# Kernel tuning notes

Hardware: AMD Instinct MI355X
Metric: run time of the kernel (lower is better)

The kernel has to match this reference:

```python
import jax, jax.numpy as jnp
import numpy as np

D = 1024
HEAD_DIM = D // 16  # attention_heads=16, used only for the softmax scale


def setup_inputs() -> dict:
    key = jax.random.key(0)
    ks = jax.random.split(key, 9)
    s = 1.0 / np.sqrt(D)
    return {
        "features": jax.random.normal(ks[0], (4, 2048, D), dtype=jnp.float32),
        "Wq": jax.random.normal(ks[1], (D, D), dtype=jnp.float32) * s,
        "bq": jnp.zeros((D,), dtype=jnp.float32),
        "Wk": jax.random.normal(ks[2], (D, D), dtype=jnp.float32) * s,
        "bk": jnp.zeros((D,), dtype=jnp.float32),
        "Wv": jax.random.normal(ks[3], (D, D), dtype=jnp.float32) * s,
        "bv": jnp.zeros((D,), dtype=jnp.float32),
        "Wo": jax.random.normal(ks[4], (D, D), dtype=jnp.float32) * s,
        "bo": jnp.zeros((D,), dtype=jnp.float32),
    }


def reference(features, Wq, bq, Wk, bk, Wv, bv, Wo, bo):
    # torch nn.Linear: x @ W.T + b
    q = features @ Wq.T + bq  # [B, S, D]
    k = features @ Wk.T + bk
    v = features @ Wv.T + bv
    scale = 1.0 / np.sqrt(HEAD_DIM).astype(np.float32)
    scores = jnp.einsum("bsd,btd->bst", q, k) * scale  # [B, S, S]
    weights = jax.nn.softmax(scores, axis=-1)
    out = jnp.einsum("bst,btd->bsd", weights, v)
    return out @ Wo.T + bo
```

## Files before the change

kernel.cpp:

```cpp
#include <hip/hip_runtime.h>


using u16 = unsigned short;
typedef __bf16 bf16x8 __attribute__((ext_vector_type(8)));
typedef float f32x4 __attribute__((ext_vector_type(4)));

__device__ inline u16 f2bf(float f) {
  union { float f; unsigned int u; } c; c.f = f;
  unsigned int u = c.u;
  u += 0x7fffu + ((u >> 16) & 1u);
  return (u16)(u >> 16);
}

__global__ __launch_bounds__(256) void cast_all(
    const float4* __restrict__ feat, const float4* __restrict__ wq,
    const float4* __restrict__ wk, const float4* __restrict__ wv,
    const float4* __restrict__ wo, ushort4* __restrict__ xbf,
    ushort4* __restrict__ wcat, float* __restrict__ lsum) {
  const int b = blockIdx.x, tx = threadIdx.x;
  if (b >= 12288) {
    lsum[(b - 12288) * 256 + tx] = 0.f;
    return;
  }
  const float4* src; ushort4* dst; int idx;
  if (b < 8192) { src = feat; dst = xbf; idx = b * 256 + tx; }
  else {
    const int w = (b - 8192) >> 10, loc = ((b - 8192) & 1023) * 256 + tx;
    src = (w == 0) ? wq : (w == 1) ? wk : (w == 2) ? wv : wo;
    dst = wcat + w * 262144; idx = loc;
  }
  float4 v = src[idx];
  ushort4 o;
  o.x = f2bf(v.x); o.y = f2bf(v.y); o.z = f2bf(v.z); o.w = f2bf(v.w);
  dst[idx] = o;
}

template <int MODE>
__global__ __launch_bounds__(256) void gemm_bt(
    const u16* __restrict__ A, const u16* __restrict__ Bm, void* __restrict__ C,
    void* __restrict__ C2, void* __restrict__ C3,
    const float* __restrict__ bias, const float* __restrict__ bias2,
    const float* __restrict__ bias3, float* __restrict__ lsum,
    int M, int N, int K, int lda, int ldc,
    float scale,
    long long sA, long long sB, long long sC)
{
  __shared__ u16 As[128 * 64];
  __shared__ u16 Bs[128 * 64];
  const int tx = threadIdx.x;
  const int wave = tx >> 6, lane = tx & 63;
  const int wm = (wave >> 1) * 64, wn = (wave & 1) * 64;
  const int m0 = blockIdx.y * 128, n0 = blockIdx.x * 128;
  const u16* Ab = A + blockIdx.z * sA + (long long)m0 * lda;
  const u16* Bb = Bm + blockIdx.z * sB + (long long)n0 * K;

  f32x4 acc[4][4] = {};

  int rT[4], qT[4];
#pragma unroll
  for (int t = 0; t < 4; ++t) {
    rT[t] = t * 32 + wave * 8 + (lane >> 3);
    qT[t] = (((lane & 7) - rT[t]) & 7) << 3;
  }
  const int ldsT[4] = {wave * 512, 2048 + wave * 512, 4096 + wave * 512,
                       6144 + wave * 512};

  const int fr = lane & 15, fq = lane >> 4;

  for (int k0 = 0; k0 < K; k0 += 64) {
#pragma unroll
    for (int t = 0; t < 4; ++t) {
      __builtin_amdgcn_global_load_lds(
          (const __attribute__((address_space(1))) void*)(Ab + (long long)rT[t] * lda + k0 + qT[t]),
          (__attribute__((address_space(3))) void*)(As + ldsT[t]), 16, 0, 0);
      __builtin_amdgcn_global_load_lds(
          (const __attribute__((address_space(1))) void*)(Bb + (long long)rT[t] * K + k0 + qT[t]),
          (__attribute__((address_space(3))) void*)(Bs + ldsT[t]), 16, 0, 0);
    }
    __syncthreads();

#pragma unroll
    for (int s = 0; s < 2; ++s) {
      bf16x8 af[4], bfv[4];
#pragma unroll
      for (int i = 0; i < 4; ++i) {
        const int Ra = wm + i * 16 + fr;
        const int Rb = wn + i * 16 + fr;
        af[i]  = *(const bf16x8*)(As + Ra * 64 + (((s * 4 + fq + Ra) & 7) << 3));
        bfv[i] = *(const bf16x8*)(Bs + Rb * 64 + (((s * 4 + fq + Rb) & 7) << 3));
      }
#pragma unroll
      for (int i = 0; i < 4; ++i)
#pragma unroll
        for (int j = 0; j < 4; ++j)
          acc[i][j] = __builtin_amdgcn_mfma_f32_16x16x32_bf16(af[i], bfv[j], acc[i][j], 0, 0, 0);
    }
    __syncthreads();
  }

  const int col = lane & 15, rq = (lane >> 4) << 2;
  const long long zC = (long long)blockIdx.z * sC;

  if constexpr (MODE == 5) {
    float rsum[4][4] = {};
#pragma unroll
    for (int i = 0; i < 4; ++i) {
#pragma unroll
      for (int j = 0; j < 4; ++j) {
        const int gn = n0 + wn + j * 16 + col;
#pragma unroll
        for (int r = 0; r < 4; ++r) {
          const int gm = m0 + wm + i * 16 + rq + r;
          const float e = __expf(acc[i][j][r] * scale);
          ((u16*)C)[zC + (long long)gm * ldc + gn] = f2bf(e);
          rsum[i][r] += e;
        }
      }
    }
#pragma unroll
    for (int i = 0; i < 4; ++i) {
#pragma unroll
      for (int r = 0; r < 4; ++r) {
        float s = rsum[i][r];
        s += __shfl_xor(s, 1); s += __shfl_xor(s, 2);
        s += __shfl_xor(s, 4); s += __shfl_xor(s, 8);
        if (col == 0)
          atomicAdd(&lsum[(long long)blockIdx.z * 2048 + m0 + wm + i * 16 + rq + r], s);
      }
    }
  } else if constexpr (MODE == 4) {
    float inv[4][4];
#pragma unroll
    for (int i = 0; i < 4; ++i)
#pragma unroll
      for (int r = 0; r < 4; ++r)
        inv[i][r] = 1.0f / lsum[(long long)blockIdx.z * 2048 + m0 + wm + i * 16 + rq + r];
#pragma unroll
    for (int i = 0; i < 4; ++i)
#pragma unroll
      for (int j = 0; j < 4; ++j) {
        const int gn = n0 + wn + j * 16 + col;
#pragma unroll
        for (int r = 0; r < 4; ++r) {
          const int gm = m0 + wm + i * 16 + rq + r;
          ((u16*)C)[zC + (long long)gm * ldc + gn] = f2bf(acc[i][j][r] * inv[i][r]);
        }
      }
  } else if constexpr (MODE == 3) {
    const int sect = n0 >> 10;
#pragma unroll
    for (int i = 0; i < 4; ++i) {
#pragma unroll
      for (int j = 0; j < 4; ++j) {
        const int gn = n0 + wn + j * 16 + col;
        const int nb = gn & 1023;
        const float bv = (sect == 0) ? bias[nb] : (sect == 1) ? bias2[nb] : bias3[nb];
#pragma unroll
        for (int r = 0; r < 4; ++r) {
          const int gm = m0 + wm + i * 16 + rq + r;
          const float v = acc[i][j][r] + bv;
          if (sect == 0) {
            ((u16*)C)[(long long)gm * 1024 + nb] = f2bf(v);
          } else if (sect == 1) {
            ((u16*)C2)[(long long)gm * 1024 + nb] = f2bf(v);
          } else {
            const int bb = gm >> 11, t = gm & 2047;
            ((u16*)C3)[((long long)bb << 21) + (long long)nb * 2048 + t] = f2bf(v);
          }
        }
      }
    }
  } else {
#pragma unroll
    for (int i = 0; i < 4; ++i) {
#pragma unroll
      for (int j = 0; j < 4; ++j) {
        const int gn = n0 + wn + j * 16 + col;
        const float bv = bias[gn];
#pragma unroll
        for (int r = 0; r < 4; ++r) {
          const int gm = m0 + wm + i * 16 + rq + r;
          ((float*)C)[zC + (long long)gm * ldc + gn] = acc[i][j][r] + bv;
        }
      }
    }
  }
}

extern "C" void kernel_launch(void* const* d_in, const int* in_sizes, int n_in,
                              void* d_out, int out_size, void* d_ws, size_t ws_size,
                              hipStream_t stream) {
  (void)in_sizes; (void)n_in; (void)out_size; (void)ws_size;
  const float* feat = (const float*)d_in[0];
  const float* Wq = (const float*)d_in[1];
  const float* bq = (const float*)d_in[2];
  const float* Wk = (const float*)d_in[3];
  const float* bk = (const float*)d_in[4];
  const float* Wv = (const float*)d_in[5];
  const float* bv = (const float*)d_in[6];
  const float* Wo = (const float*)d_in[7];
  const float* bo = (const float*)d_in[8];
  float* out = (float*)d_out;

  char* ws = (char*)d_ws;
  const unsigned long long MB = 1024ull * 1024ull;
  u16* Xbf  = (u16*)(ws);
  u16* Wcat = (u16*)(ws + 16 * MB);
  u16* Wob  = Wcat + 3ll * 1024 * 1024;
  u16* Q    = (u16*)(ws + 24 * MB);
  u16* Kbuf = (u16*)(ws + 40 * MB);
  u16* Vt   = (u16*)(ws + 56 * MB);
  u16* P    = (u16*)(ws + 72 * MB);
  float* lsum = (float*)(ws + 104 * MB);
  u16* attn = Q;

  dim3 blk(256);

  cast_all<<<12320, blk, 0, stream>>>((const float4*)feat, (const float4*)Wq,
                                      (const float4*)Wk, (const float4*)Wv,
                                      (const float4*)Wo, (ushort4*)Xbf,
                                      (ushort4*)Wcat, lsum);

  gemm_bt<3><<<dim3(24, 64, 1), blk, 0, stream>>>(
      Xbf, Wcat, Q, Kbuf, Vt, bq, bk, bv, nullptr,
      8192, 3072, 1024, 1024, 0, 1.f, 0, 0, 0);

  gemm_bt<5><<<dim3(16, 16, 4), blk, 0, stream>>>(
      Q, Kbuf, P, nullptr, nullptr, nullptr, nullptr, nullptr, lsum,
      2048, 2048, 1024, 1024, 2048, 0.125f,
      2048ll * 1024, 2048ll * 1024, 2048ll * 2048);

  gemm_bt<4><<<dim3(8, 16, 4), blk, 0, stream>>>(
      P, Vt, attn, nullptr, nullptr, nullptr, nullptr, nullptr, lsum,
      2048, 1024, 2048, 2048, 1024, 1.f,
      2048ll * 2048, 1024ll * 2048, 2048ll * 1024);

  gemm_bt<2><<<dim3(8, 64, 1), blk, 0, stream>>>(
      attn, Wob, out, nullptr, nullptr, bo, nullptr, nullptr, nullptr,
      8192, 1024, 1024, 1024, 1024, 1.f, 0, 0, 0);
}
```

Baseline: 307.9 us.

## Rewrite GEMM as 8-wave 256-row tiles with double-buffered LDS prefetch

Replaces the 128x128 single-buffer GEMM with a 512-thread kernel that computes 256xBN tiles (BN 256 or 128 per call). Global-to-LDS loads are double buffered, with the next tiles' loads issued in quarters between MFMA phases and fenced by explicit vmcnt waits and barriers. MFMA sections run at raised wave priority. The aim is to hide global load latency behind compute and raise data reuse per block, at the cost of more LDS and registers per block and fewer blocks for the smaller attention GEMMs.

After: 346.0 us. 1.12x slower.

```diff
diff --git a/kernel.cpp b/kernel.cpp
--- a/kernel.cpp
+++ b/kernel.cpp
@@ -4,6 +4,9 @@
 using u16 = unsigned short;
 typedef __bf16 bf16x8 __attribute__((ext_vector_type(8)));
 typedef float f32x4 __attribute__((ext_vector_type(4)));
+
+#define AS1 __attribute__((address_space(1)))
+#define AS3 __attribute__((address_space(3)))
 
 __device__ inline u16 f2bf(float f) {
   union { float f; unsigned int u; } c; c.f = f;
@@ -35,153 +38,190 @@
   dst[idx] = o;
 }
 
-template <int MODE>
-__global__ __launch_bounds__(256) void gemm_bt(
+template <int MODE, int BN>
+__global__ __launch_bounds__(512, 2) void gemm8p(
     const u16* __restrict__ A, const u16* __restrict__ Bm, void* __restrict__ C,
     void* __restrict__ C2, void* __restrict__ C3,
     const float* __restrict__ bias, const float* __restrict__ bias2,
     const float* __restrict__ bias3, float* __restrict__ lsum,
-    int M, int N, int K, int lda, int ldc,
-    float scale,
+    int M, int N, int K, int lda, int ldc, float scale,
     long long sA, long long sB, long long sC)
 {
-  __shared__ u16 As[128 * 64];
-  __shared__ u16 Bs[128 * 64];
+  constexpr int NL  = BN / 128;
+  constexpr int NFH = BN / 128;
+  constexpr int NH  = BN / 2;
+  constexpr int NW  = NH / 4;
+
+  __shared__ u16 As[2 * 256 * 64];
+  __shared__ u16 Bs[2 * BN * 64];
+
   const int tx = threadIdx.x;
   const int wave = tx >> 6, lane = tx & 63;
-  const int wm = (wave >> 1) * 64, wn = (wave & 1) * 64;
-  const int m0 = blockIdx.y * 128, n0 = blockIdx.x * 128;
+  const int wm = wave >> 2, wn = wave & 3;
+  const int fr = lane & 15, fq = lane >> 4;
+  const int lr = lane >> 3, lp = lane & 7;
+  const int m0 = blockIdx.y * 256, n0 = blockIdx.x * BN;
   const u16* Ab = A + blockIdx.z * sA + (long long)m0 * lda;
   const u16* Bb = Bm + blockIdx.z * sB + (long long)n0 * K;
-
-  f32x4 acc[4][4] = {};
-
-  int rT[4], qT[4];
-#pragma unroll
-  for (int t = 0; t < 4; ++t) {
-    rT[t] = t * 32 + wave * 8 + (lane >> 3);
-    qT[t] = (((lane & 7) - rT[t]) & 7) << 3;
-  }
-  const int ldsT[4] = {wave * 512, 2048 + wave * 512, 4096 + wave * 512,
-                       6144 + wave * 512};
-
-  const int fr = lane & 15, fq = lane >> 4;
-
-  for (int k0 = 0; k0 < K; k0 += 64) {
-#pragma unroll
-    for (int t = 0; t < 4; ++t) {
+  const int NT = K >> 6;
+
+  f32x4 acc[8][2 * NFH] = {};
+
+  auto stageA = [&](int t, int h) {
+#pragma unroll
+    for (int s = 0; s < 2; ++s) {
+      const int R = h * 128 + wave * 16 + s * 8 + lr;
+      const int q = (lp - R) & 7;
       __builtin_amdgcn_global_load_lds(
-          (const __attribute__((address_space(1))) void*)(Ab + (long long)rT[t] * lda + k0 + qT[t]),
-          (__attribute__((address_space(3))) void*)(As + ldsT[t]), 16, 0, 0);
+          (const AS1 void*)(Ab + (long long)R * lda + t * 64 + q * 8),
+          (AS3 void*)(As + (t & 1) * 16384 + (h * 128 + wave * 16 + s * 8) * 64),
+          16, 0, 0);
+    }
+  };
+  auto stageB = [&](int t, int h) {
+#pragma unroll
+    for (int s = 0; s < NL; ++s) {
+      const int R = h * NH + wave * (8 * NL) + s * 8 + lr;
+      const int q = (lp - R) & 7;
       __builtin_amdgcn_global_load_lds(
-          (const __attribute__((address_space(1))) void*)(Bb + (long long)rT[t] * K + k0 + qT[t]),
-          (__attribute__((address_space(3))) void*)(Bs + ldsT[t]), 16, 0, 0);
-    }
-    __syncthreads();
-
-#pragma unroll
-    for (int s = 0; s < 2; ++s) {
-      bf16x8 af[4], bfv[4];
-#pragma unroll
-      for (int i = 0; i < 4; ++i) {
-        const int Ra = wm + i * 16 + fr;
-        const int Rb = wn + i * 16 + fr;
-        af[i]  = *(const bf16x8*)(As + Ra * 64 + (((s * 4 + fq + Ra) & 7) << 3));
-        bfv[i] = *(const bf16x8*)(Bs + Rb * 64 + (((s * 4 + fq + Rb) & 7) << 3));
-      }
-#pragma unroll
-      for (int i = 0; i < 4; ++i)
-#pragma unroll
-        for (int j = 0; j < 4; ++j)
-          acc[i][j] = __builtin_amdgcn_mfma_f32_16x16x32_bf16(af[i], bfv[j], acc[i][j], 0, 0, 0);
-    }
-    __syncthreads();
+          (const AS1 void*)(Bb + (long long)R * K + t * 64 + q * 8),
+          (AS3 void*)(Bs + (t & 1) * (BN * 64) + (h * NH + wave * (8 * NL) + s * 8) * 64),
+          16, 0, 0);
+    }
+  };
+
+  stageA(0, 0); stageA(0, 1); stageB(0, 0); stageB(0, 1);
+  stageA(1, 0); stageB(1, 0);
+  if constexpr (BN == 256) asm volatile("s_waitcnt vmcnt(4)" ::: "memory");
+  else                     asm volatile("s_waitcnt vmcnt(3)" ::: "memory");
+  __builtin_amdgcn_s_barrier();
+
+  for (int t = 0; t < NT; ++t) {
+    const u16* At = As + (t & 1) * 16384;
+    const u16* Bt = Bs + (t & 1) * (BN * 64);
+#pragma unroll
+    for (int qp = 0; qp < 4; ++qp) {
+      const int h = qp >> 1, g = qp & 1;
+      bf16x8 af[4][2], bv[NFH][2];
+#pragma unroll
+      for (int fi = 0; fi < 4; ++fi) {
+        const int R = h * 128 + wm * 64 + fi * 16 + fr;
+#pragma unroll
+        for (int s = 0; s < 2; ++s)
+          af[fi][s] = *(const bf16x8*)(At + R * 64 + (((s * 4 + fq + R) & 7) << 3));
+      }
+#pragma unroll
+      for (int fj = 0; fj < NFH; ++fj) {
+        const int R = g * NH + wn * NW + fj * 16 + fr;
+#pragma unroll
+        for (int s = 0; s < 2; ++s)
+          bv[fj][s] = *(const bf16x8*)(Bt + R * 64 + (((s * 4 + fq + R) & 7) << 3));
+      }
+      if (qp == 0)      { if (t + 1 < NT) stageA(t + 1, 1); }
+      else if (qp == 1) { if (t + 1 < NT) stageB(t + 1, 1); }
+      else if (qp == 2) { if (t + 2 < NT) stageA(t + 2, 0); }
+      else              { if (t + 2 < NT) stageB(t + 2, 0); }
+
+      __builtin_amdgcn_s_barrier();
+      asm volatile("s_waitcnt lgkmcnt(0)" ::: "memory");
+      __builtin_amdgcn_sched_barrier(0);
+      __builtin_amdgcn_s_setprio(1);
+#pragma unroll
+      for (int s = 0; s < 2; ++s)
+#pragma unroll
+        for (int fi = 0; fi < 4; ++fi)
+#pragma unroll
+          for (int fj = 0; fj < NFH; ++fj)
+            acc[h * 4 + fi][g * NFH + fj] = __builtin_amdgcn_mfma_f32_16x16x32_bf16(
+                af[fi][s], bv[fj][s], acc[h * 4 + fi][g * NFH + fj], 0, 0, 0);
+      __builtin_amdgcn_s_setprio(0);
+      if (qp == 3) {
+        if constexpr (BN == 256) asm volatile("s_waitcnt vmcnt(4)" ::: "memory");
+        else                     asm volatile("s_waitcnt vmcnt(3)" ::: "memory");
+      }
+      __builtin_amdgcn_s_barrier();
+    }
   }
 
   const int col = lane & 15, rq = (lane >> 4) << 2;
   const long long zC = (long long)blockIdx.z * sC;
 
   if constexpr (MODE == 5) {
-    float rsum[4][4] = {};
-#pragma unroll
-    for (int i = 0; i < 4; ++i) {
-#pragma unroll
-      for (int j = 0; j < 4; ++j) {
-        const int gn = n0 + wn + j * 16 + col;
+#pragma unroll
+    for (int i = 0; i < 8; ++i) {
+      const int gmb = m0 + (i >> 2) * 128 + wm * 64 + (i & 3) * 16 + rq;
+      float rs[4] = {0.f, 0.f, 0.f, 0.f};
+#pragma unroll
+      for (int j = 0; j < 2 * NFH; ++j) {
+        const int gn = n0 + (j / NFH) * NH + wn * NW + (j % NFH) * 16 + col;
 #pragma unroll
         for (int r = 0; r < 4; ++r) {
-          const int gm = m0 + wm + i * 16 + rq + r;
           const float e = __expf(acc[i][j][r] * scale);
-          ((u16*)C)[zC + (long long)gm * ldc + gn] = f2bf(e);
-          rsum[i][r] += e;
+          ((u16*)C)[zC + (long long)(gmb + r) * ldc + gn] = f2bf(e);
+          rs[r] += e;
         }
       }
-    }
-#pragma unroll
-    for (int i = 0; i < 4; ++i) {
 #pragma unroll
       for (int r = 0; r < 4; ++r) {
-        float s = rsum[i][r];
+        float s = rs[r];
         s += __shfl_xor(s, 1); s += __shfl_xor(s, 2);
         s += __shfl_xor(s, 4); s += __shfl_xor(s, 8);
         if (col == 0)
-          atomicAdd(&lsum[(long long)blockIdx.z * 2048 + m0 + wm + i * 16 + rq + r], s);
+          atomicAdd(&lsum[(long long)blockIdx.z * 2048 + gmb + r], s);
       }
     }
   } else if constexpr (MODE == 4) {
-    float inv[4][4];
-#pragma unroll
-    for (int i = 0; i < 4; ++i)
+#pragma unroll
+    for (int i = 0; i < 8; ++i) {
+      const int gmb = m0 + (i >> 2) * 128 + wm * 64 + (i & 3) * 16 + rq;
+      float inv[4];
 #pragma unroll
       for (int r = 0; r < 4; ++r)
-        inv[i][r] = 1.0f / lsum[(long long)blockIdx.z * 2048 + m0 + wm + i * 16 + rq + r];
-#pragma unroll
-    for (int i = 0; i < 4; ++i)
-#pragma unroll
-      for (int j = 0; j < 4; ++j) {
-        const int gn = n0 + wn + j * 16 + col;
-#pragma unroll
-        for (int r = 0; r < 4; ++r) {
-          const int gm = m0 + wm + i * 16 + rq + r;
-          ((u16*)C)[zC + (long long)gm * ldc + gn] = f2bf(acc[i][j][r] * inv[i][r]);
-        }
-      }
+        inv[r] = 1.0f / lsum[(long long)blockIdx.z * 2048 + gmb + r];
+#pragma unroll
+      for (int j = 0; j < 2 * NFH; ++j) {
+        const int gn = n0 + (j / NFH) * NH + wn * NW + (j % NFH) * 16 + col;
+#pragma unroll
+        for (int r = 0; r < 4; ++r)
+          ((u16*)C)[zC + (long long)(gmb + r) * ldc + gn] = f2bf(acc[i][j][r] * inv[r]);
+      }
+    }
   } else if constexpr (MODE == 3) {
     const int sect = n0 >> 10;
 #pragma unroll
-    for (int i = 0; i < 4; ++i) {
-#pragma unroll
-      for (int j = 0; j < 4; ++j) {
-        const int gn = n0 + wn + j * 16 + col;
+    for (int i = 0; i < 8; ++i) {
+      const int gmb = m0 + (i >> 2) * 128 + wm * 64 + (i & 3) * 16 + rq;
+#pragma unroll
+      for (int j = 0; j < 2 * NFH; ++j) {
+        const int gn = n0 + (j / NFH) * NH + wn * NW + (j % NFH) * 16 + col;
         const int nb = gn & 1023;
-        const float bv = (sect == 0) ? bias[nb] : (sect == 1) ? bias2[nb] : bias3[nb];
+        const float bvv = (sect == 0) ? bias[nb] : (sect == 1) ? bias2[nb] : bias3[nb];
 #pragma unroll
         for (int r = 0; r < 4; ++r) {
-          const int gm = m0 + wm + i * 16 + rq + r;
-          const float v = acc[i][j][r] + bv;
+          const int gm = gmb + r;
+          const float v = acc[i][j][r] + bvv;
           if (sect == 0) {
             ((u16*)C)[(long long)gm * 1024 + nb] = f2bf(v);
           } else if (sect == 1) {
             ((u16*)C2)[(long long)gm * 1024 + nb] = f2bf(v);
           } else {
-            const int bb = gm >> 11, t = gm & 2047;
-            ((u16*)C3)[((long long)bb << 21) + (long long)nb * 2048 + t] = f2bf(v);
+            const int bb = gm >> 11, tt = gm & 2047;
+            ((u16*)C3)[((long long)bb << 21) + (long long)nb * 2048 + tt] = f2bf(v);
           }
         }
       }
     }
   } else {
 #pragma unroll
-    for (int i = 0; i < 4; ++i) {
-#pragma unroll
-      for (int j = 0; j < 4; ++j) {
-        const int gn = n0 + wn + j * 16 + col;
-        const float bv = bias[gn];
-#pragma unroll
-        for (int r = 0; r < 4; ++r) {
-          const int gm = m0 + wm + i * 16 + rq + r;
-          ((float*)C)[zC + (long long)gm * ldc + gn] = acc[i][j][r] + bv;
-        }
+    for (int i = 0; i < 8; ++i) {
+      const int gmb = m0 + (i >> 2) * 128 + wm * 64 + (i & 3) * 16 + rq;
+#pragma unroll
+      for (int j = 0; j < 2 * NFH; ++j) {
+        const int gn = n0 + (j / NFH) * NH + wn * NW + (j % NFH) * 16 + col;
+        const float bvv = bias[gn];
+#pragma unroll
+        for (int r = 0; r < 4; ++r)
+          ((float*)C)[zC + (long long)(gmb + r) * ldc + gn] = acc[i][j][r] + bvv;
       }
     }
   }
@@ -214,28 +254,26 @@
   float* lsum = (float*)(ws + 104 * MB);
   u16* attn = Q;
 
-  dim3 blk(256);
-
-  cast_all<<<12320, blk, 0, stream>>>((const float4*)feat, (const float4*)Wq,
+  cast_all<<<12320, 256, 0, stream>>>((const float4*)feat, (const float4*)Wq,
                                       (const float4*)Wk, (const float4*)Wv,
                                       (const float4*)Wo, (ushort4*)Xbf,
                                       (ushort4*)Wcat, lsum);
 
-  gemm_bt<3><<<dim3(24, 64, 1), blk, 0, stream>>>(
+  gemm8p<3, 256><<<dim3(12, 32, 1), 512, 0, stream>>>(
       Xbf, Wcat, Q, Kbuf, Vt, bq, bk, bv, nullptr,
       8192, 3072, 1024, 1024, 0, 1.f, 0, 0, 0);
 
-  gemm_bt<5><<<dim3(16, 16, 4), blk, 0, stream>>>(
+  gemm8p<5, 256><<<dim3(8, 8, 4), 512, 0, stream>>>(
       Q, Kbuf, P, nullptr, nullptr, nullptr, nullptr, nullptr, lsum,
       2048, 2048, 1024, 1024, 2048, 0.125f,
       2048ll * 1024, 2048ll * 1024, 2048ll * 2048);
 
-  gemm_bt<4><<<dim3(8, 16, 4), blk, 0, stream>>>(
+  gemm8p<4, 128><<<dim3(8, 8, 4), 512, 0, stream>>>(
       P, Vt, attn, nullptr, nullptr, nullptr, nullptr, nullptr, lsum,
       2048, 1024, 2048, 2048, 1024, 1.f,
       2048ll * 2048, 1024ll * 2048, 2048ll * 1024);
 
-  gemm_bt<2><<<dim3(8, 64, 1), blk, 0, stream>>>(
+  gemm8p<2, 128><<<dim3(8, 32, 1), 512, 0, stream>>>(
       attn, Wob, out, nullptr, nullptr, bo, nullptr, nullptr, nullptr,
       8192, 1024, 1024, 1024, 1024, 1.f, 0, 0, 0);
 }
```

## Double-buffer LDS tiles in GEMM to overlap global loads with MFMA

Applied to the files above, without the earlier changes.

Shared-memory tiles become two ping-pong buffers, so the next K-slice is fetched with global_load_lds while MFMAs run on the current slice. The second barrier per iteration is removed, and wave priority is raised around the MFMA section. This is meant to hide global load latency, in exchange for doubling LDS use to 64KB per block, which may lower occupancy. There is a possible hazard: the next load into a buffer is issued right after the barrier, with no explicit lgkmcnt wait covering the LDS reads of the previous iteration.

New measurement: 310.2 us. No clear change (+0.7%).

```diff
diff --git a/kernel.cpp b/kernel.cpp
--- a/kernel.cpp
+++ b/kernel.cpp
@@ -4,6 +4,9 @@
 using u16 = unsigned short;
 typedef __bf16 bf16x8 __attribute__((ext_vector_type(8)));
 typedef float f32x4 __attribute__((ext_vector_type(4)));
+
+#define AS1 __attribute__((address_space(1)))
+#define AS3 __attribute__((address_space(3)))
 
 __device__ inline u16 f2bf(float f) {
   union { float f; unsigned int u; } c; c.f = f;
@@ -45,8 +48,8 @@
     float scale,
     long long sA, long long sB, long long sC)
 {
-  __shared__ u16 As[128 * 64];
-  __shared__ u16 Bs[128 * 64];
+  __shared__ u16 As[2 * 128 * 64];
+  __shared__ u16 Bs[2 * 128 * 64];
   const int tx = threadIdx.x;
   const int wave = tx >> 6, lane = tx & 63;
   const int wm = (wave >> 1) * 64, wn = (wave & 1) * 64;
@@ -67,18 +70,29 @@
 
   const int fr = lane & 15, fq = lane >> 4;
 
-  for (int k0 = 0; k0 < K; k0 += 64) {
+  auto stage = [&](int k0, int buf) {
 #pragma unroll
     for (int t = 0; t < 4; ++t) {
       __builtin_amdgcn_global_load_lds(
-          (const __attribute__((address_space(1))) void*)(Ab + (long long)rT[t] * lda + k0 + qT[t]),
-          (__attribute__((address_space(3))) void*)(As + ldsT[t]), 16, 0, 0);
+          (const AS1 void*)(Ab + (long long)rT[t] * lda + k0 + qT[t]),
+          (AS3 void*)(As + buf * 8192 + ldsT[t]), 16, 0, 0);
       __builtin_amdgcn_global_load_lds(
-          (const __attribute__((address_space(1))) void*)(Bb + (long long)rT[t] * K + k0 + qT[t]),
-          (__attribute__((address_space(3))) void*)(Bs + ldsT[t]), 16, 0, 0);
-    }
-    __syncthreads();
-
+          (const AS1 void*)(Bb + (long long)rT[t] * K + k0 + qT[t]),
+          (AS3 void*)(Bs + buf * 8192 + ldsT[t]), 16, 0, 0);
+    }
+  };
+
+  stage(0, 0);
+  asm volatile("s_waitcnt vmcnt(0)" ::: "memory");
+  __builtin_amdgcn_s_barrier();
+
+  int cur = 0;
+  for (int k0 = 0; k0 < K; k0 += 64) {
+    if (k0 + 64 < K) stage(k0 + 64, cur ^ 1);
+
+    const u16* Ac = As + cur * 8192;
+    const u16* Bc = Bs + cur * 8192;
+    __builtin_amdgcn_s_setprio(1);
 #pragma unroll
     for (int s = 0; s < 2; ++s) {
       bf16x8 af[4], bfv[4];
@@ -86,8 +100,8 @@
       for (int i = 0; i < 4; ++i) {
         const int Ra = wm + i * 16 + fr;
         const int Rb = wn + i * 16 + fr;
-        af[i]  = *(const bf16x8*)(As + Ra * 64 + (((s * 4 + fq + Ra) & 7) << 3));
-        bfv[i] = *(const bf16x8*)(Bs + Rb * 64 + (((s * 4 + fq + Rb) & 7) << 3));
+        af[i]  = *(const bf16x8*)(Ac + Ra * 64 + (((s * 4 + fq + Ra) & 7) << 3));
+        bfv[i] = *(const bf16x8*)(Bc + Rb * 64 + (((s * 4 + fq + Rb) & 7) << 3));
       }
 #pragma unroll
       for (int i = 0; i < 4; ++i)
@@ -95,7 +109,11 @@
         for (int j = 0; j < 4; ++j)
           acc[i][j] = __builtin_amdgcn_mfma_f32_16x16x32_bf16(af[i], bfv[j], acc[i][j], 0, 0, 0);
     }
-    __syncthreads();
+    __builtin_amdgcn_s_setprio(0);
+
+    asm volatile("s_waitcnt vmcnt(0)" ::: "memory");
+    __builtin_amdgcn_s_barrier();
+    cur ^= 1;
   }
 
   const int col = lane & 15, rq = (lane >> 4) << 2;
```
